# Kernel optimization log

Hardware: AMD Instinct MI355X
Metric: run time of the kernel (lower is better)

The kernel has to match this reference:

```python
import jax, jax.numpy as jnp
import numpy as np
from jax import lax


def setup_inputs() -> dict:
    key = jax.random.key(0)
    k1, k2, k3, k4 = jax.random.split(key, 4)
    D = 128
    B = 16
    image = jax.random.normal(k1, (1, D, D, D), jnp.float32)          # [1, D, H, W]
    x = jax.random.normal(k2, (B, 1, D, D, D), jnp.float32)           # [B, 1, D, H, W]
    # Conv3d(1, 27, kernel_size=3) parameters
    W = jax.random.normal(k3, (27, 1, 3, 3, 3), jnp.float32) * (1.0 / np.sqrt(27.0))
    b = jax.random.normal(k4, (27,), jnp.float32) * 0.01
    return {"image": image, "x": x, "W": W, "b": b}


def reference(image, x, W, b):
    D, H, Wd = image.shape[1], image.shape[2], image.shape[3]
    # K = Conv3d(image): per-voxel 27 filter taps. Unbatched CDHW -> add batch dim.
    K = lax.conv_general_dilated(
        image[None], W, window_strides=(1, 1, 1), padding='SAME',
        dimension_numbers=('NCDHW', 'OIDHW', 'NCDHW'))[0]             # [27, D, H, W]
    K = K + b[:, None, None, None]
    # permute (1,2,3,0) + unflatten(3,(3,3,3)) -> [D, H, W, 3, 3, 3]
    K = jnp.moveaxis(K, 0, -1).reshape(D, H, Wd, 3, 3, 3)
    # Apply dynamic per-voxel 3x3x3 filter: sum of 27 shifted slices
    xp = jnp.pad(x, ((0, 0), (0, 0), (1, 1), (1, 1), (1, 1)))         # [B,1,D+2,H+2,W+2]
    y = jnp.zeros_like(x)
    for di in range(3):
        for dj in range(3):
            for dk in range(3):
                tap = K[..., di, dj, dk][None, None]                  # [1,1,D,H,W]
                y = y + tap * xp[:, :, di:di + D, dj:dj + H, dk:dk + Wd]
    return y
```

## Files before the change

kernel.cpp:

```cpp
#include <hip/hip_runtime.h>

typedef __fp16 f16x2 __attribute__((ext_vector_type(2)));

#define Dm 128
#define Bn 16
#define VOX (Dm * Dm * Dm)
#define NT 256
#define WR 19
#define SLAB 589
#define NSL 9

__device__ __forceinline__ int iclamp(int v, int lo, int hi) {
  return v < lo ? lo : (v > hi ? hi : v);
}
__device__ __forceinline__ f16x2 pkrtz(float lo, float hi) {
  return __builtin_amdgcn_cvt_pkrtz(lo, hi);
}
__device__ __forceinline__ float pkbits(float lo, float hi) {
  return __builtin_bit_cast(float, __builtin_amdgcn_cvt_pkrtz(lo, hi));
}
__device__ __forceinline__ f16x2 asf16x2(float w) {
  return __builtin_bit_cast(f16x2, w);
}
__device__ __forceinline__ f16x2 midpair(f16x2 P, f16x2 Q) {
  unsigned r = __builtin_amdgcn_perm(__builtin_bit_cast(unsigned, P),
                                     __builtin_bit_cast(unsigned, Q),
                                     0x05040302u);
  return __builtin_bit_cast(f16x2, r);
}

extern "C" __global__ void packW(const float* __restrict__ Wf,
                                 const float* __restrict__ bfp,
                                 float* __restrict__ wpk) {
  int i = threadIdx.x;
  if (i < 729) {
    int o = i / 27, t = i - o * 27;
    float v = Wf[i];
    wpk[t * 27 + o] = pkbits(v, v);
  } else if (i < 756) {
    float b = bfp[i - 729];
    wpk[i] = pkbits(b, b);
  }
}

__device__ __forceinline__ void load_batch(float2 nx[NSL], const float* xb,
                                           const int off[NSL]) {
#pragma unroll
  for (int k = 0; k < NSL; ++k) nx[k] = *(const float2*)(xb + off[k]);
}
__device__ __forceinline__ void stage_lds(float* sxw, const float2 nx[NSL],
                                          int lane) {
#pragma unroll
  for (int k = 0; k < NSL; ++k)
    sxw[64 * k + lane] = pkbits(nx[k].x, nx[k].y);
}

__device__ __forceinline__ void apply_tile4(const float* sxw,
                                            const f16x2* KA, const f16x2* KB,
                                            int ty, int tx,
                                            f16x2& outA, f16x2& outB) {
  f16x2 aAa = {(__fp16)0.f, (__fp16)0.f}, aAb = aAa;
  f16x2 aBa = aAa, aBb = aAa;
#pragma unroll
  for (int rr = 0; rr < 9; ++rr) {
    const int idx = ((rr / 3) * 10 + ty + (rr % 3)) * WR + 2 * tx;
    float u0 = sxw[idx], u1 = sxw[idx + 1], u2 = sxw[idx + 2], u3 = sxw[idx + 3];
    f16x2 h1 = asf16x2(u1), h2 = asf16x2(u2);
    f16x2 m01 = midpair(h1, asf16x2(u0));
    f16x2 m12 = midpair(h2, h1);
    f16x2 m23 = midpair(asf16x2(u3), h2);
    if (rr & 1) {
      aAb = __builtin_elementwise_fma(KA[rr * 3 + 0], m01, aAb);
      aAb = __builtin_elementwise_fma(KA[rr * 3 + 1], h1,  aAb);
      aAb = __builtin_elementwise_fma(KA[rr * 3 + 2], m12, aAb);
      aBb = __builtin_elementwise_fma(KB[rr * 3 + 0], m12, aBb);
      aBb = __builtin_elementwise_fma(KB[rr * 3 + 1], h2,  aBb);
      aBb = __builtin_elementwise_fma(KB[rr * 3 + 2], m23, aBb);
    } else {
      aAa = __builtin_elementwise_fma(KA[rr * 3 + 0], m01, aAa);
      aAa = __builtin_elementwise_fma(KA[rr * 3 + 1], h1,  aAa);
      aAa = __builtin_elementwise_fma(KA[rr * 3 + 2], m12, aAa);
      aBa = __builtin_elementwise_fma(KB[rr * 3 + 0], m12, aBa);
      aBa = __builtin_elementwise_fma(KB[rr * 3 + 1], h2,  aBa);
      aBa = __builtin_elementwise_fma(KB[rr * 3 + 2], m23, aBa);
    }
  }
  outA = aAa + aAb;
  outB = aBa + aBb;
}

extern "C" __global__ void __launch_bounds__(NT, 4)
fused3d(const float* __restrict__ img, const float* __restrict__ x,
        const float* __restrict__ wpk, float* __restrict__ out)
{
  __shared__ float sX0[4][SLAB];
  __shared__ float sX1[4][SLAB];

  const int tid  = threadIdx.x;
  const int lane = tid & 63;
  const int wv   = tid >> 6;
  const int tx   = lane & 7;
  const int ty   = lane >> 3;

  const int bid = blockIdx.x;
  const int s  = (bid & 7) * 256 + (bid >> 3);
  const int bx = s & 3, by = (s >> 2) & 15, bz = s >> 6;
  const int w0 = bx * 32, h0 = by * 8, d0 = bz * 4;

  int off[NSL];
  float mk0[NSL], mk1[NSL];
#pragma unroll
  for (int k = 0; k < NSL; ++k) {
    int i  = 64 * k + lane;
    int r  = i / WR;
    int c  = i - r * WR;
    int zz = r / 10;
    int yy = r - zz * 10;
    int gdo = d0 + wv + zz - 1;
    int gho = h0 + yy - 1;
    int gwo = w0 - 2 + 2 * c;
    int gd = iclamp(gdo, 0, Dm - 1);
    int gh = iclamp(gho, 0, Dm - 1);
    int gw = iclamp(gwo, 0, Dm - 2);
    off[k] = (gd * Dm + gh) * Dm + gw;
    bool rk = ((unsigned)gdo < Dm) & ((unsigned)gho < Dm) & (zz < 3);
    mk0[k] = (rk & ((unsigned)gwo < Dm))       ? 1.f : 0.f;
    mk1[k] = (rk & ((unsigned)(gwo + 1) < Dm)) ? 1.f : 0.f;
  }

  float* sx0 = sX0[wv];
  float* sx1 = sX1[wv];

  float2 nxA[NSL], nxB[NSL];
  load_batch(nxA, x, off);
#pragma unroll
  for (int k = 0; k < NSL; ++k) {
    float2 v = *(const float2*)(img + off[k]);
    sx0[64 * k + lane] = pkbits(v.x * mk0[k], v.y * mk1[k]);
  }

  f16x2 KA[27], KB[27];
#pragma unroll
  for (int o = 0; o < 27; ++o) { KA[o] = asf16x2(wpk[729 + o]); KB[o] = KA[o]; }
#pragma unroll
  for (int rr = 0; rr < 9; ++rr) {
    const int idx = ((rr / 3) * 10 + ty + (rr % 3)) * WR + 2 * tx;
    float u0 = sx0[idx], u1 = sx0[idx + 1], u2 = sx0[idx + 2], u3 = sx0[idx + 3];
    f16x2 h1 = asf16x2(u1), h2 = asf16x2(u2);
    f16x2 m01 = midpair(h1, asf16x2(u0));
    f16x2 m12 = midpair(h2, h1);
    f16x2 m23 = midpair(asf16x2(u3), h2);
    const float* wA = wpk + (rr * 3 + 0) * 27;
    const float* wB = wpk + (rr * 3 + 1) * 27;
    const float* wC = wpk + (rr * 3 + 2) * 27;
#pragma unroll
    for (int o = 0; o < 27; ++o) {
      f16x2 wa = asf16x2(wA[o]), wb = asf16x2(wB[o]), wc = asf16x2(wC[o]);
      KA[o] = __builtin_elementwise_fma(wa, m01, KA[o]);
      KA[o] = __builtin_elementwise_fma(wb, h1,  KA[o]);
      KA[o] = __builtin_elementwise_fma(wc, m12, KA[o]);
      KB[o] = __builtin_elementwise_fma(wa, m12, KB[o]);
      KB[o] = __builtin_elementwise_fma(wb, h2,  KB[o]);
      KB[o] = __builtin_elementwise_fma(wc, m23, KB[o]);
    }
  }

  const int od = d0 + wv, oh = h0 + ty, ow = w0 + 4 * tx;
#pragma unroll
  for (int o = 0; o < 27; ++o) {
    const int di = o / 9, dj = (o / 3) % 3, dk = o % 3;
    const bool mm = ((unsigned)(od + di - 1) < Dm) & ((unsigned)(oh + dj - 1) < Dm);
    const float a0 = (mm & ((unsigned)(ow + dk - 1) < Dm)) ? 1.f : 0.f;
    const float a1 = (mm & ((unsigned)(ow + dk)     < Dm)) ? 1.f : 0.f;
    const float b0 = (mm & ((unsigned)(ow + dk + 1) < Dm)) ? 1.f : 0.f;
    const float b1 = (mm & ((unsigned)(ow + dk + 2) < Dm)) ? 1.f : 0.f;
    KA[o] *= pkrtz(a0, a1);
    KB[o] *= pkrtz(b0, b1);
  }

  const size_t obase = (((size_t)od) * Dm + oh) * Dm + ow;

#pragma unroll 1
  for (int bb = 0; bb < Bn; bb += 2) {
    stage_lds(sx1, nxA, lane);
    load_batch(nxB, x + (size_t)(bb + 1) * VOX, off);
    {
      f16x2 oA, oB;
      apply_tile4(sx1, KA, KB, ty, tx, oA, oB);
      float4 st; st.x = (float)oA.x; st.y = (float)oA.y;
      st.z = (float)oB.x; st.w = (float)oB.y;
      *(float4*)&out[(size_t)bb * VOX + obase] = st;
    }
    stage_lds(sx0, nxB, lane);
    if (bb + 2 < Bn) load_batch(nxA, x + (size_t)(bb + 2) * VOX, off);
    {
      f16x2 oA, oB;
      apply_tile4(sx0, KA, KB, ty, tx, oA, oB);
      float4 st; st.x = (float)oA.x; st.y = (float)oA.y;
      st.z = (float)oB.x; st.w = (float)oB.y;
      *(float4*)&out[(size_t)(bb + 1) * VOX + obase] = st;
    }
  }
}

extern "C" void kernel_launch(void* const* d_in, const int* in_sizes, int n_in,
                              void* d_out, int out_size, void* d_ws, size_t ws_size,
                              hipStream_t stream) {
  const float* img = (const float*)d_in[0];
  const float* x   = (const float*)d_in[1];
  const float* Wf  = (const float*)d_in[2];
  const float* bf  = (const float*)d_in[3];
  float* out = (float*)d_out;
  float* wpk = (float*)d_ws;
  hipLaunchKernelGGL(packW, dim3(1), dim3(768), 0, stream, Wf, bf, wpk);
  hipLaunchKernelGGL(fused3d, dim3(2048), dim3(NT), 0, stream, img, x, wpk, out);
}
```

Before: 133.5 us.

## Pack two batches per f16x2 lane and load image taps directly from global

Restages x into LDS with the two halves of each packed f16x2 holding the same voxel from two different batch elements, so each FMA computes one voxel for two batches. Kernel taps use broadcast (duplo/duphi) weights, which removes the midpair permutes, and only one LDS buffer is used, with two batches loaded per iteration. The image conv for the per-voxel filter now reads global memory directly instead of staging through LDS. The trade-offs are more register pressure from holding two prefetched batches, possible LDS bank conflicts from the 38-word row stride, and uncoalesced scalar global reads for the image.

```diff
diff --git a/kernel.cpp b/kernel.cpp
--- a/kernel.cpp
+++ b/kernel.cpp
@@ -6,9 +6,9 @@
 #define Bn 16
 #define VOX (Dm * Dm * Dm)
 #define NT 256
-#define WR 19
-#define SLAB 589
-#define NSL 9
+#define RSTR 38
+#define SLAB 1216
+#define NPS 9
 
 __device__ __forceinline__ int iclamp(int v, int lo, int hi) {
   return v < lo ? lo : (v > hi ? hi : v);
@@ -22,11 +22,14 @@
 __device__ __forceinline__ f16x2 asf16x2(float w) {
   return __builtin_bit_cast(f16x2, w);
 }
-__device__ __forceinline__ f16x2 midpair(f16x2 P, f16x2 Q) {
-  unsigned r = __builtin_amdgcn_perm(__builtin_bit_cast(unsigned, P),
-                                     __builtin_bit_cast(unsigned, Q),
-                                     0x05040302u);
-  return __builtin_bit_cast(f16x2, r);
+__device__ __forceinline__ f16x2 duplo(f16x2 v) {
+  return __builtin_shufflevector(v, v, 0, 0);
+}
+__device__ __forceinline__ f16x2 duphi(f16x2 v) {
+  return __builtin_shufflevector(v, v, 1, 1);
+}
+__device__ __forceinline__ void keep(float& a) {
+  asm volatile("" : "+v"(a));
 }
 
 extern "C" __global__ void packW(const float* __restrict__ Wf,
@@ -43,58 +46,11 @@
   }
 }
 
-__device__ __forceinline__ void load_batch(float2 nx[NSL], const float* xb,
-                                           const int off[NSL]) {
-#pragma unroll
-  for (int k = 0; k < NSL; ++k) nx[k] = *(const float2*)(xb + off[k]);
-}
-__device__ __forceinline__ void stage_lds(float* sxw, const float2 nx[NSL],
-                                          int lane) {
-#pragma unroll
-  for (int k = 0; k < NSL; ++k)
-    sxw[64 * k + lane] = pkbits(nx[k].x, nx[k].y);
-}
-
-__device__ __forceinline__ void apply_tile4(const float* sxw,
-                                            const f16x2* KA, const f16x2* KB,
-                                            int ty, int tx,
-                                            f16x2& outA, f16x2& outB) {
-  f16x2 aAa = {(__fp16)0.f, (__fp16)0.f}, aAb = aAa;
-  f16x2 aBa = aAa, aBb = aAa;
-#pragma unroll
-  for (int rr = 0; rr < 9; ++rr) {
-    const int idx = ((rr / 3) * 10 + ty + (rr % 3)) * WR + 2 * tx;
-    float u0 = sxw[idx], u1 = sxw[idx + 1], u2 = sxw[idx + 2], u3 = sxw[idx + 3];
-    f16x2 h1 = asf16x2(u1), h2 = asf16x2(u2);
-    f16x2 m01 = midpair(h1, asf16x2(u0));
-    f16x2 m12 = midpair(h2, h1);
-    f16x2 m23 = midpair(asf16x2(u3), h2);
-    if (rr & 1) {
-      aAb = __builtin_elementwise_fma(KA[rr * 3 + 0], m01, aAb);
-      aAb = __builtin_elementwise_fma(KA[rr * 3 + 1], h1,  aAb);
-      aAb = __builtin_elementwise_fma(KA[rr * 3 + 2], m12, aAb);
-      aBb = __builtin_elementwise_fma(KB[rr * 3 + 0], m12, aBb);
-      aBb = __builtin_elementwise_fma(KB[rr * 3 + 1], h2,  aBb);
-      aBb = __builtin_elementwise_fma(KB[rr * 3 + 2], m23, aBb);
-    } else {
-      aAa = __builtin_elementwise_fma(KA[rr * 3 + 0], m01, aAa);
-      aAa = __builtin_elementwise_fma(KA[rr * 3 + 1], h1,  aAa);
-      aAa = __builtin_elementwise_fma(KA[rr * 3 + 2], m12, aAa);
-      aBa = __builtin_elementwise_fma(KB[rr * 3 + 0], m12, aBa);
-      aBa = __builtin_elementwise_fma(KB[rr * 3 + 1], h2,  aBa);
-      aBa = __builtin_elementwise_fma(KB[rr * 3 + 2], m23, aBa);
-    }
-  }
-  outA = aAa + aAb;
-  outB = aBa + aBb;
-}
-
 extern "C" __global__ void __launch_bounds__(NT, 4)
 fused3d(const float* __restrict__ img, const float* __restrict__ x,
         const float* __restrict__ wpk, float* __restrict__ out)
 {
-  __shared__ float sX0[4][SLAB];
-  __shared__ float sX1[4][SLAB];
+  __shared__ float sX[4][SLAB];
 
   const int tid  = threadIdx.x;
   const int lane = tid & 63;
@@ -107,36 +63,31 @@
   const int bx = s & 3, by = (s >> 2) & 15, bz = s >> 6;
   const int w0 = bx * 32, h0 = by * 8, d0 = bz * 4;
 
-  int off[NSL];
-  float mk0[NSL], mk1[NSL];
-#pragma unroll
-  for (int k = 0; k < NSL; ++k) {
-    int i  = 64 * k + lane;
-    int r  = i / WR;
-    int c  = i - r * WR;
+  const int od = d0 + wv, oh = h0 + ty, ow = w0 + 4 * tx;
+
+  int goff[NPS], lofs[NPS];
+#pragma unroll
+  for (int k = 0; k < NPS; ++k) {
+    int j  = 64 * k + lane;
+    int r  = j / 18;
+    int pc = j - r * 18;
     int zz = r / 10;
     int yy = r - zz * 10;
-    int gdo = d0 + wv + zz - 1;
-    int gho = h0 + yy - 1;
-    int gwo = w0 - 2 + 2 * c;
-    int gd = iclamp(gdo, 0, Dm - 1);
-    int gh = iclamp(gho, 0, Dm - 1);
-    int gw = iclamp(gwo, 0, Dm - 2);
-    off[k] = (gd * Dm + gh) * Dm + gw;
-    bool rk = ((unsigned)gdo < Dm) & ((unsigned)gho < Dm) & (zz < 3);
-    mk0[k] = (rk & ((unsigned)gwo < Dm))       ? 1.f : 0.f;
-    mk1[k] = (rk & ((unsigned)(gwo + 1) < Dm)) ? 1.f : 0.f;
-  }
-
-  float* sx0 = sX0[wv];
-  float* sx1 = sX1[wv];
-
-  float2 nxA[NSL], nxB[NSL];
-  load_batch(nxA, x, off);
-#pragma unroll
-  for (int k = 0; k < NSL; ++k) {
-    float2 v = *(const float2*)(img + off[k]);
-    sx0[64 * k + lane] = pkbits(v.x * mk0[k], v.y * mk1[k]);
+    int gd = iclamp(d0 + wv + zz - 1, 0, Dm - 1);
+    int gh = iclamp(h0 + yy - 1, 0, Dm - 1);
+    int gw = iclamp(w0 - 2 + 2 * pc, 0, Dm - 2);
+    goff[k] = (gd * Dm + gh) * Dm + gw;
+    lofs[k] = r * RSTR + 2 * pc;
+  }
+
+  float* sl = sX[wv];
+
+  float2 nb[NPS], nc[NPS];
+#pragma unroll
+  for (int k = 0; k < NPS; ++k) {
+    nb[k] = *(const float2*)(x + goff[k]);
+    nc[k] = *(const float2*)(x + VOX + goff[k]);
+    keep(nb[k].x); keep(nb[k].y); keep(nc[k].x); keep(nc[k].y);
   }
 
   f16x2 KA[27], KB[27];
@@ -144,28 +95,35 @@
   for (int o = 0; o < 27; ++o) { KA[o] = asf16x2(wpk[729 + o]); KB[o] = KA[o]; }
 #pragma unroll
   for (int rr = 0; rr < 9; ++rr) {
-    const int idx = ((rr / 3) * 10 + ty + (rr % 3)) * WR + 2 * tx;
-    float u0 = sx0[idx], u1 = sx0[idx + 1], u2 = sx0[idx + 2], u3 = sx0[idx + 3];
-    f16x2 h1 = asf16x2(u1), h2 = asf16x2(u2);
-    f16x2 m01 = midpair(h1, asf16x2(u0));
-    f16x2 m12 = midpair(h2, h1);
-    f16x2 m23 = midpair(asf16x2(u3), h2);
+    const int zz = rr / 3, dy = rr % 3;
+    const int gd0 = od + zz - 1, gh0 = oh + dy - 1;
+    const bool rk = ((unsigned)gd0 < Dm) & ((unsigned)gh0 < Dm);
+    const float* rp = img + ((size_t)iclamp(gd0, 0, Dm - 1) * Dm
+                             + iclamp(gh0, 0, Dm - 1)) * Dm;
+    float v[6];
+#pragma unroll
+    for (int c = 0; c < 6; ++c) {
+      int gw = ow + c - 1;
+      v[c] = (rk & ((unsigned)gw < Dm)) ? rp[iclamp(gw, 0, Dm - 1)] : 0.f;
+    }
+    f16x2 mA0 = pkrtz(v[0], v[1]), mA1 = pkrtz(v[1], v[2]);
+    f16x2 mA2 = pkrtz(v[2], v[3]);
+    f16x2 mB1 = pkrtz(v[3], v[4]), mB2 = pkrtz(v[4], v[5]);
     const float* wA = wpk + (rr * 3 + 0) * 27;
     const float* wB = wpk + (rr * 3 + 1) * 27;
     const float* wC = wpk + (rr * 3 + 2) * 27;
 #pragma unroll
     for (int o = 0; o < 27; ++o) {
       f16x2 wa = asf16x2(wA[o]), wb = asf16x2(wB[o]), wc = asf16x2(wC[o]);
-      KA[o] = __builtin_elementwise_fma(wa, m01, KA[o]);
-      KA[o] = __builtin_elementwise_fma(wb, h1,  KA[o]);
-      KA[o] = __builtin_elementwise_fma(wc, m12, KA[o]);
-      KB[o] = __builtin_elementwise_fma(wa, m12, KB[o]);
-      KB[o] = __builtin_elementwise_fma(wb, h2,  KB[o]);
-      KB[o] = __builtin_elementwise_fma(wc, m23, KB[o]);
-    }
-  }
-
-  const int od = d0 + wv, oh = h0 + ty, ow = w0 + 4 * tx;
+      KA[o] = __builtin_elementwise_fma(wa, mA0, KA[o]);
+      KA[o] = __builtin_elementwise_fma(wb, mA1, KA[o]);
+      KA[o] = __builtin_elementwise_fma(wc, mA2, KA[o]);
+      KB[o] = __builtin_elementwise_fma(wa, mA2, KB[o]);
+      KB[o] = __builtin_elementwise_fma(wb, mB1, KB[o]);
+      KB[o] = __builtin_elementwise_fma(wc, mB2, KB[o]);
+    }
+  }
+
 #pragma unroll
   for (int o = 0; o < 27; ++o) {
     const int di = o / 9, dj = (o / 3) % 3, dk = o % 3;
@@ -179,27 +137,62 @@
   }
 
   const size_t obase = (((size_t)od) * Dm + oh) * Dm + ow;
+  const int rbase = 4 * tx;
 
 #pragma unroll 1
-  for (int bb = 0; bb < Bn; bb += 2) {
-    stage_lds(sx1, nxA, lane);
-    load_batch(nxB, x + (size_t)(bb + 1) * VOX, off);
-    {
-      f16x2 oA, oB;
-      apply_tile4(sx1, KA, KB, ty, tx, oA, oB);
-      float4 st; st.x = (float)oA.x; st.y = (float)oA.y;
-      st.z = (float)oB.x; st.w = (float)oB.y;
-      *(float4*)&out[(size_t)bb * VOX + obase] = st;
-    }
-    stage_lds(sx0, nxB, lane);
-    if (bb + 2 < Bn) load_batch(nxA, x + (size_t)(bb + 2) * VOX, off);
-    {
-      f16x2 oA, oB;
-      apply_tile4(sx0, KA, KB, ty, tx, oA, oB);
-      float4 st; st.x = (float)oA.x; st.y = (float)oA.y;
-      st.z = (float)oB.x; st.w = (float)oB.y;
-      *(float4*)&out[(size_t)(bb + 1) * VOX + obase] = st;
-    }
+  for (int pp = 0; pp < Bn / 2; ++pp) {
+#pragma unroll
+    for (int k = 0; k < NPS; ++k) {
+      float2 wp;
+      wp.x = pkbits(nb[k].x, nc[k].x);
+      wp.y = pkbits(nb[k].y, nc[k].y);
+      *(float2*)&sl[lofs[k]] = wp;
+    }
+
+    if (pp + 1 < Bn / 2) {
+      const float* xb = x + (size_t)(2 * pp + 2) * VOX;
+#pragma unroll
+      for (int k = 0; k < NPS; ++k) {
+        nb[k] = *(const float2*)(xb + goff[k]);
+        nc[k] = *(const float2*)(xb + VOX + goff[k]);
+        keep(nb[k].x); keep(nb[k].y); keep(nc[k].x); keep(nc[k].y);
+      }
+    }
+
+    f16x2 acc0 = {(__fp16)0.f, (__fp16)0.f};
+    f16x2 acc1 = acc0, acc2 = acc0, acc3 = acc0;
+#pragma unroll
+    for (int rr = 0; rr < 9; ++rr) {
+      const int row  = (rr / 3) * 10 + ty + (rr % 3);
+      const int base = row * RSTR + rbase;
+      float2 qa = *(const float2*)&sl[base];
+      float2 qb = *(const float2*)&sl[base + 2];
+      float2 qc = *(const float2*)&sl[base + 4];
+      float2 qd = *(const float2*)&sl[base + 6];
+      f16x2 U1 = asf16x2(qa.y);
+      f16x2 U2 = asf16x2(qb.x);
+      f16x2 U3 = asf16x2(qb.y);
+      f16x2 U4 = asf16x2(qc.x);
+      f16x2 U5 = asf16x2(qc.y);
+      f16x2 U6 = asf16x2(qd.x);
+      f16x2 Uv[6] = {U1, U2, U3, U4, U5, U6};
+#pragma unroll
+      for (int dk = 0; dk < 3; ++dk) {
+        const int t = rr * 3 + dk;
+        acc0 = __builtin_elementwise_fma(duplo(KA[t]), Uv[0 + dk], acc0);
+        acc1 = __builtin_elementwise_fma(duphi(KA[t]), Uv[1 + dk], acc1);
+        acc2 = __builtin_elementwise_fma(duplo(KB[t]), Uv[2 + dk], acc2);
+        acc3 = __builtin_elementwise_fma(duphi(KB[t]), Uv[3 + dk], acc3);
+      }
+    }
+
+    float4 s0, s1;
+    s0.x = (float)acc0.x; s0.y = (float)acc1.x;
+    s0.z = (float)acc2.x; s0.w = (float)acc3.x;
+    s1.x = (float)acc0.y; s1.y = (float)acc1.y;
+    s1.z = (float)acc2.y; s1.w = (float)acc3.y;
+    *(float4*)&out[(size_t)(2 * pp)     * VOX + obase] = s0;
+    *(float4*)&out[(size_t)(2 * pp + 1) * VOX + obase] = s1;
   }
 }
 
```

Result: slower. 436.3 us (+226.9%).
